# Kernel tuning notes

Hardware: AMD Instinct MI355X
Metric: run time of the kernel (lower is better)

The kernel has to match this reference:

```python
import jax, jax.numpy as jnp
import numpy as np

N = 100000
E = 1600000
D = 64        # HID_NODE_ENC == HID_EDGE_ENC
H = 128       # HIDDEN_NODE_ONE
EPS = 1e-5
NEG_SLOPE = 0.01


def _xavier(key, shape):
    fan_in, fan_out = shape[0], shape[1]
    limit = float(np.sqrt(6.0 / (fan_in + fan_out)))
    return jax.random.uniform(key, shape, jnp.float32, -limit, limit)


def setup_inputs() -> dict:
    key = jax.random.key(0)
    ks = jax.random.split(key, 10)
    x = jax.random.normal(ks[0], (N, D), jnp.float32)
    edge_index = jax.random.randint(ks[1], (2, E), 0, N, jnp.int64)
    edge_attr = jax.random.normal(ks[2], (E, D), jnp.float32)
    u = jax.random.normal(ks[3], (1, 16), jnp.float32)
    batch = jnp.zeros((N,), jnp.int64)
    b_init = jnp.float32(0.01)
    params = {
        # node_mlp_1: Lin(128->128), LeakyReLU, BN(128), Lin(128->128)
        "W1": _xavier(ks[4], (2 * D, H)), "b1": jnp.full((H,), b_init),
        "g1": jnp.ones((H,), jnp.float32), "be1": jnp.zeros((H,), jnp.float32),
        "W2": _xavier(ks[5], (H, H)), "b2": jnp.full((H,), b_init),
        # node_mlp_2: Lin(192->128), LeakyReLU, BN(128), Lin(128->64)
        "W3": _xavier(ks[6], (H + D, H)), "b3": jnp.full((H,), b_init),
        "g2": jnp.ones((H,), jnp.float32), "be2": jnp.zeros((H,), jnp.float32),
        "W4": _xavier(ks[7], (H, D)), "b4": jnp.full((D,), b_init),
    }
    return {"x": x, "edge_index": edge_index, "edge_attr": edge_attr,
            "u": u, "batch": batch, **params}


def _bn(h, gamma, beta):
    # BatchNorm1d in training mode: biased batch statistics
    mean = jnp.mean(h, axis=0)
    var = jnp.mean(jnp.square(h - mean), axis=0)
    return (h - mean) * jax.lax.rsqrt(var + EPS) * gamma + beta


def reference(x, edge_index, edge_attr, u, batch,
              W1, b1, g1, be1, W2, b2,
              W3, b3, g2, be2, W4, b4):
    row, col = edge_index[0], edge_index[1]
    # gather + concat: [E, 2D]
    h = jnp.concatenate([x[row], edge_attr], axis=1)
    # node_mlp_1
    h = jax.nn.leaky_relu(h @ W1 + b1, NEG_SLOPE)
    h = _bn(h, g1, be1)
    h = h @ W2 + b2                       # [E, H]
    # scatter_add by destination node
    agg = jax.ops.segment_sum(h, col, num_segments=x.shape[0])  # [N, H]
    # concat with node feats, node_mlp_2
    h2 = jnp.concatenate([x, agg], axis=1)  # [N, H+D]
    h2 = jax.nn.leaky_relu(h2 @ W3 + b3, NEG_SLOPE)
    h2 = _bn(h2, g2, be2)
    return h2 @ W4 + b4                    # [N, D]
```

## Files before the change

### kernel.cpp

```cpp
#include <hip/hip_runtime.h>

#define NN 100000
#define NE 1600000
#define NTILE_E (NE / 128)
#define NTILE_N 782

typedef __attribute__((ext_vector_type(4))) float f32x4;
typedef __attribute__((ext_vector_type(8))) short s16x8;

__device__ __forceinline__ unsigned short f2bf(float f) {
  unsigned u = __builtin_bit_cast(unsigned, f);
  u = (u + 0x7FFFu + ((u >> 16) & 1u)) >> 16;
  return (unsigned short)u;
}
__device__ __forceinline__ void pack4(float4 v, unsigned short* dst) {
  ushort4 h;
  h.x = f2bf(v.x); h.y = f2bf(v.y); h.z = f2bf(v.z); h.w = f2bf(v.w);
  *(ushort4*)dst = h;
}

__global__ void k0_prep(const float* __restrict__ W1, const float* __restrict__ W3,
                        unsigned short* __restrict__ W1bT, unsigned short* __restrict__ W3bT) {
  int i = blockIdx.x * 256 + threadIdx.x;
  if (i < 16384) {
    int n = i >> 7, k = i & 127;
    W1bT[i] = f2bf(W1[k * 128 + n]);
  } else if (i < 16384 + 24576) {
    int j = i - 16384;
    int n = j / 192, k = j % 192;
    W3bT[j] = f2bf(W3[k * 128 + n]);
  }
}

__global__ void k_hist(const int* __restrict__ eidx, int* __restrict__ hist) {
  int e = blockIdx.x * 256 + threadIdx.x;
  if (e < NE) atomicAdd(&hist[eidx[NE + e]], 1);
}

__global__ void k_scan(int* __restrict__ hist, float* __restrict__ cntF) {
  __shared__ int ssum[1024];
  const int t = threadIdx.x;
  const int base = t * 98;
  const int cl = (base >= NN) ? 0 : ((NN - base < 98) ? (NN - base) : 98);
  int s = 0;
  for (int i = 0; i < cl; i++) s += hist[base + i];
  ssum[t] = s;
  __syncthreads();
  for (int d = 1; d < 1024; d <<= 1) {
    int v = (t >= d) ? ssum[t - d] : 0;
    __syncthreads();
    ssum[t] += v;
    __syncthreads();
  }
  int run = (t == 0) ? 0 : ssum[t - 1];
  for (int i = 0; i < cl; i++) {
    int hv = hist[base + i];
    hist[base + i] = run;
    cntF[base + i] = (float)hv;
    run += hv;
  }
}

__global__ void k_scatter(const int* __restrict__ eidx, int* __restrict__ off,
                          int* __restrict__ colS, int* __restrict__ eaIdx) {
  int e = blockIdx.x * 256 + threadIdx.x;
  if (e < NE) {
    int c = eidx[NE + e];
    int p = atomicAdd(&off[c], 1);
    colS[p] = c;
    eaIdx[p] = e;
  }
}

__global__ __launch_bounds__(256, 2) void k1_edge(
    const float* __restrict__ x, const int* __restrict__ eidx,
    const float* __restrict__ ea, const unsigned short* __restrict__ W1bT,
    const float* __restrict__ b1, const int* __restrict__ colS,
    const int* __restrict__ eaIdx,
    float* __restrict__ S, float* __restrict__ stat1) {
  __shared__ __align__(16) unsigned short At[128][136];
  __shared__ __align__(16) float Hs1[128][68];
  __shared__ int rIdxS[128];
  __shared__ int eIdxS[128];
  __shared__ int colT[132];
  __shared__ float sred[256];
  float (*Hs0)[68] = (float (*)[68])At;

  const int tid = threadIdx.x;
  const int wave = tid >> 6, lane = tid & 63;
  const int l15 = lane & 15, quad = lane >> 4;
  const int rowbase = (wave >> 1) * 64;
  const int colbase = (wave & 1) * 64;

  s16x8 bfrag[4][4];
#pragma unroll
  for (int ct = 0; ct < 4; ct++)
#pragma unroll
    for (int ks = 0; ks < 4; ks++)
      bfrag[ct][ks] = *(const s16x8*)(W1bT + (colbase + ct * 16 + l15) * 128 + ks * 32 + quad * 8);

  float b1j[4];
#pragma unroll
  for (int ct = 0; ct < 4; ct++) b1j[ct] = b1[colbase + ct * 16 + l15];

  float lsum[4] = {0, 0, 0, 0}, lsq[4] = {0, 0, 0, 0};

  for (int tile = blockIdx.x; tile < NTILE_E; tile += gridDim.x) {
    const int eb = tile * 128;
    __syncthreads();
    if (tid < 128) {
      int e0 = eaIdx[eb + tid];
      eIdxS[tid] = e0;
      rIdxS[tid] = eidx[e0];
      colT[tid + 1] = colS[eb + tid];
    } else if (tid == 128) {
      colT[0] = (eb > 0) ? colS[eb - 1] : -1;
    } else if (tid == 129) {
      colT[129] = (eb + 128 < NE) ? colS[eb + 128] : -1;
    }
    __syncthreads();
#pragma unroll
    for (int i = 0; i < 8; i++) {
      int idx = tid + i * 256; int e = idx >> 4, c = idx & 15;
      float4 v = ((const float4*)x)[(size_t)rIdxS[e] * 16 + c];
      pack4(v, &At[e][c * 4]);
    }
#pragma unroll
    for (int i = 0; i < 8; i++) {
      int idx = tid + i * 256; int e = idx >> 4, c = idx & 15;
      float4 v = ((const float4*)ea)[(size_t)eIdxS[e] * 16 + c];
      pack4(v, &At[e][64 + c * 4]);
    }
    __syncthreads();

    f32x4 acc[4][4];
#pragma unroll
    for (int rt = 0; rt < 4; rt++)
#pragma unroll
      for (int ct = 0; ct < 4; ct++) acc[rt][ct] = (f32x4){0.f, 0.f, 0.f, 0.f};

#pragma unroll
    for (int ks = 0; ks < 4; ks++) {
      s16x8 af[4];
#pragma unroll
      for (int rt = 0; rt < 4; rt++)
        af[rt] = *(const s16x8*)&At[rowbase + rt * 16 + l15][ks * 32 + quad * 8];
#pragma unroll
      for (int rt = 0; rt < 4; rt++)
#pragma unroll
        for (int ct = 0; ct < 4; ct++)
          acc[rt][ct] = __builtin_amdgcn_mfma_f32_16x16x32_bf16(af[rt], bfrag[ct][ks], acc[rt][ct], 0, 0, 0);
    }

    __syncthreads();
    {
      float (*H)[68] = (wave & 1) ? Hs1 : Hs0;
#pragma unroll
      for (int rt = 0; rt < 4; rt++)
#pragma unroll
        for (int r = 0; r < 4; r++) {
          const int er = rowbase + rt * 16 + quad * 4 + r;
#pragma unroll
          for (int ct = 0; ct < 4; ct++) {
            float v = acc[rt][ct][r] + b1j[ct];
            v = v > 0.0f ? v : 0.01f * v;
            lsum[ct] += v; lsq[ct] += v * v;
            H[er][ct * 16 + l15] = v;
          }
        }
    }
    __syncthreads();

    {
      const int col = tid & 63;
      const int r0 = (tid >> 6) * 32;
#pragma unroll
      for (int h = 0; h < 2; h++) {
        float (*H)[68] = h ? Hs1 : Hs0;
        float runsum = H[r0][col];
        int runstart = r0;
        int curnode = colT[r0 + 1];
        for (int r = r0 + 1; r < r0 + 32; ++r) {
          int nd = colT[r + 1];
          float v = H[r][col];
          if (nd == curnode) { runsum += v; }
          else {
            float* p = S + (size_t)curnode * 128 + h * 64 + col;
            if (colT[runstart] != curnode) *p = runsum;
            else atomicAdd(p, runsum);
            curnode = nd; runsum = v; runstart = r;
          }
        }
        float* p = S + (size_t)curnode * 128 + h * 64 + col;
        if (colT[runstart] != curnode && colT[r0 + 33] != curnode) *p = runsum;
        else atomicAdd(p, runsum);
      }
    }
  }

  sred[tid] = 0.0f;
  __syncthreads();
#pragma unroll
  for (int ct = 0; ct < 4; ct++) {
    float s = lsum[ct], q = lsq[ct];
    s += __shfl_down(s, 32); q += __shfl_down(q, 32);
    s += __shfl_down(s, 16); q += __shfl_down(q, 16);
    if (lane < 16) {
      atomicAdd(&sred[colbase + ct * 16 + l15], s);
      atomicAdd(&sred[128 + colbase + ct * 16 + l15], q);
    }
  }
  __syncthreads();
  atomicAdd(&stat1[tid], sred[tid]);
}

__global__ void k2_fold1(const float* __restrict__ stat1, const float* __restrict__ g1,
                         const float* __restrict__ be1, const float* __restrict__ W2,
                         const float* __restrict__ b2,
                         unsigned short* __restrict__ W2pT, float* __restrict__ v128) {
  __shared__ float s1s[128], t1s[128];
  __shared__ float red[256];
  const int tid = threadIdx.x;
  if (tid < 128) {
    float mean = stat1[tid] * (1.0f / NE);
    float var = stat1[128 + tid] * (1.0f / NE) - mean * mean;
    float rstd = rsqrtf(var + 1e-5f);
    float s = g1[tid] * rstd;
    s1s[tid] = s; t1s[tid] = be1[tid] - mean * s;
  }
  __syncthreads();
  const int b = blockIdx.x;
  if (b < 16) {
#pragma unroll
    for (int j = 0; j < 4; j++) {
      int i = b * 1024 + j * 256 + tid;
      int k = i >> 7, n = i & 127;
      W2pT[n * 128 + k] = f2bf(s1s[k] * W2[i]);
    }
  } else {
    int j = tid & 127, hh = tid >> 7;
    float p = 0.f;
    for (int k = hh * 64; k < hh * 64 + 64; k++) p += t1s[k] * W2[k * 128 + j];
    red[tid] = p;
    __syncthreads();
    if (tid < 128) v128[tid] = red[tid] + red[tid + 128] + b2[tid];
  }
}

__global__ __launch_bounds__(256, 2) void k3_node(
    const float* __restrict__ x, const float* __restrict__ S, const float* __restrict__ cnt,
    const unsigned short* __restrict__ W2pT, const float* __restrict__ v128,
    const unsigned short* __restrict__ W3bT, const float* __restrict__ b3,
    unsigned short* __restrict__ tOut, float* __restrict__ stat2) {
  __shared__ unsigned short Abuf[128][136];
  __shared__ unsigned short Xbuf[128][72];
  __shared__ float cbuf[128];
  __shared__ float sred[256];

  const int tid = threadIdx.x;
  const int wave = tid >> 6, lane = tid & 63;
  const int l15 = lane & 15, quad = lane >> 4;
  const int rowbase = (wave >> 1) * 64;
  const int colbase = (wave & 1) * 64;

  float vj[4], b3j[4];
#pragma unroll
  for (int ct = 0; ct < 4; ct++) {
    int jc = colbase + ct * 16 + l15;
    vj[ct] = v128[jc]; b3j[ct] = b3[jc];
  }
  float lsum[4] = {0, 0, 0, 0}, lsq[4] = {0, 0, 0, 0};

  for (int t = blockIdx.x; t < NTILE_N; t += gridDim.x) {
    const int nb = t * 128;
    __syncthreads();
#pragma unroll
    for (int i = 0; i < 16; i++) {
      int idx = tid + i * 256; int e = idx >> 5, c = idx & 31;
      int node = nb + e;
      float4 v = {0.f, 0.f, 0.f, 0.f};
      if (node < NN) v = ((const float4*)S)[(size_t)node * 32 + c];
      pack4(v, &Abuf[e][c * 4]);
    }
#pragma unroll
    for (int i = 0; i < 8; i++) {
      int idx = tid + i * 256; int e = idx >> 4, c = idx & 15;
      int node = nb + e;
      float4 v = {0.f, 0.f, 0.f, 0.f};
      if (node < NN) v = ((const float4*)x)[(size_t)node * 16 + c];
      pack4(v, &Xbuf[e][c * 4]);
    }
    if (tid < 128) cbuf[tid] = (nb + tid < NN) ? cnt[nb + tid] : 0.0f;
    __syncthreads();

    f32x4 acc[4][4];
#pragma unroll
    for (int rt = 0; rt < 4; rt++)
#pragma unroll
      for (int ct = 0; ct < 4; ct++) acc[rt][ct] = (f32x4){0.f, 0.f, 0.f, 0.f};
#pragma unroll
    for (int ks = 0; ks < 4; ks++) {
      s16x8 af[4];
#pragma unroll
      for (int rt = 0; rt < 4; rt++)
        af[rt] = *(const s16x8*)&Abuf[rowbase + rt * 16 + l15][ks * 32 + quad * 8];
      s16x8 bfr[4];
#pragma unroll
      for (int ct = 0; ct < 4; ct++)
        bfr[ct] = *(const s16x8*)(W2pT + (colbase + ct * 16 + l15) * 128 + ks * 32 + quad * 8);
#pragma unroll
      for (int rt = 0; rt < 4; rt++)
#pragma unroll
        for (int ct = 0; ct < 4; ct++)
          acc[rt][ct] = __builtin_amdgcn_mfma_f32_16x16x32_bf16(af[rt], bfr[ct], acc[rt][ct], 0, 0, 0);
    }
    __syncthreads();
#pragma unroll
    for (int rt = 0; rt < 4; rt++)
#pragma unroll
      for (int r = 0; r < 4; r++) {
        int er = rowbase + rt * 16 + quad * 4 + r;
#pragma unroll
        for (int ct = 0; ct < 4; ct++) {
          float val = acc[rt][ct][r] + cbuf[er] * vj[ct];
          Abuf[er][colbase + ct * 16 + l15] = f2bf(val);
        }
      }
    __syncthreads();

    f32x4 acc2[4][4];
#pragma unroll
    for (int rt = 0; rt < 4; rt++)
#pragma unroll
      for (int ct = 0; ct < 4; ct++) acc2[rt][ct] = (f32x4){0.f, 0.f, 0.f, 0.f};
#pragma unroll
    for (int ks = 0; ks < 6; ks++) {
      s16x8 af[4];
      if (ks < 2) {
#pragma unroll
        for (int rt = 0; rt < 4; rt++)
          af[rt] = *(const s16x8*)&Xbuf[rowbase + rt * 16 + l15][ks * 32 + quad * 8];
      } else {
#pragma unroll
        for (int rt = 0; rt < 4; rt++)
          af[rt] = *(const s16x8*)&Abuf[rowbase + rt * 16 + l15][(ks - 2) * 32 + quad * 8];
      }
      s16x8 bfr[4];
#pragma unroll
      for (int ct = 0; ct < 4; ct++)
        bfr[ct] = *(const s16x8*)(W3bT + (size_t)(colbase + ct * 16 + l15) * 192 + ks * 32 + quad * 8);
#pragma unroll
      for (int rt = 0; rt < 4; rt++)
#pragma unroll
        for (int ct = 0; ct < 4; ct++)
          acc2[rt][ct] = __builtin_amdgcn_mfma_f32_16x16x32_bf16(af[rt], bfr[ct], acc2[rt][ct], 0, 0, 0);
    }

#pragma unroll
    for (int rt = 0; rt < 4; rt++)
#pragma unroll
      for (int r = 0; r < 4; r++) {
        int er = rowbase + rt * 16 + quad * 4 + r;
        int node = nb + er;
        if (node < NN) {
#pragma unroll
          for (int ct = 0; ct < 4; ct++) {
            float val = acc2[rt][ct][r] + b3j[ct];
            val = val > 0.0f ? val : 0.01f * val;
            lsum[ct] += val; lsq[ct] += val * val;
            tOut[(size_t)node * 128 + colbase + ct * 16 + l15] = f2bf(val);
          }
        }
      }
  }

  sred[tid] = 0.0f;
  __syncthreads();
#pragma unroll
  for (int ct = 0; ct < 4; ct++) {
    float s = lsum[ct], q = lsq[ct];
    s += __shfl_down(s, 32); q += __shfl_down(q, 32);
    s += __shfl_down(s, 16); q += __shfl_down(q, 16);
    if (lane < 16) {
      atomicAdd(&sred[colbase + ct * 16 + l15], s);
      atomicAdd(&sred[128 + colbase + ct * 16 + l15], q);
    }
  }
  __syncthreads();
  atomicAdd(&stat2[tid], sred[tid]);
}

__global__ void k5_fold2(const float* __restrict__ stat2, const float* __restrict__ g2,
                         const float* __restrict__ be2, const float* __restrict__ W4,
                         const float* __restrict__ b4,
                         unsigned short* __restrict__ W4fT, float* __restrict__ b4f) {
  __shared__ float s2s[128], t2s[128];
  __shared__ float red[256];
  const int tid = threadIdx.x;
  if (tid < 128) {
    float mean = stat2[tid] * (1.0f / NN);
    float var = stat2[128 + tid] * (1.0f / NN) - mean * mean;
    float rstd = rsqrtf(var + 1e-5f);
    float s = g2[tid] * rstd;
    s2s[tid] = s; t2s[tid] = be2[tid] - mean * s;
  }
  __syncthreads();
  const int b = blockIdx.x;
  if (b < 8) {
#pragma unroll
    for (int j = 0; j < 4; j++) {
      int i = b * 1024 + j * 256 + tid;
      int k = i >> 6, n = i & 63;
      W4fT[n * 128 + k] = f2bf(s2s[k] * W4[i]);
    }
  } else {
    int j = tid & 63, part = tid >> 6;
    float p = 0.f;
    for (int k = part * 32; k < part * 32 + 32; k++) p += t2s[k] * W4[k * 64 + j];
    red[tid] = p;
    __syncthreads();
    if (tid < 64) b4f[tid] = red[tid] + red[tid + 64] + red[tid + 128] + red[tid + 192] + b4[tid];
  }
}

__global__ __launch_bounds__(256, 2) void k6_out(
    const unsigned short* __restrict__ tIn, const unsigned short* __restrict__ W4fT,
    const float* __restrict__ b4f, float* __restrict__ out) {
  __shared__ unsigned short Abuf[128][136];
  const int tid = threadIdx.x;
  const int wave = tid >> 6, lane = tid & 63;
  const int l15 = lane & 15, quad = lane >> 4;
  const int rowbase = (wave >> 1) * 64;
  const int colbase = (wave & 1) * 32;

  s16x8 bfrag[2][4];
#pragma unroll
  for (int ct = 0; ct < 2; ct++)
#pragma unroll
    for (int ks = 0; ks < 4; ks++)
      bfrag[ct][ks] = *(const s16x8*)(W4fT + (colbase + ct * 16 + l15) * 128 + ks * 32 + quad * 8);
  float bj[2];
#pragma unroll
  for (int ct = 0; ct < 2; ct++) bj[ct] = b4f[colbase + ct * 16 + l15];

  for (int t = blockIdx.x; t < NTILE_N; t += gridDim.x) {
    const int nb = t * 128;
    __syncthreads();
#pragma unroll
    for (int i = 0; i < 8; i++) {
      int idx = tid + i * 256; int e = idx >> 4, c = idx & 15;
      int node = nb + e;
      s16x8 v = {0, 0, 0, 0, 0, 0, 0, 0};
      if (node < NN) v = *(const s16x8*)(tIn + (size_t)node * 128 + c * 8);
      *(s16x8*)&Abuf[e][c * 8] = v;
    }
    __syncthreads();

    f32x4 acc[4][2];
#pragma unroll
    for (int rt = 0; rt < 4; rt++)
#pragma unroll
      for (int ct = 0; ct < 2; ct++) acc[rt][ct] = (f32x4){0.f, 0.f, 0.f, 0.f};
#pragma unroll
    for (int ks = 0; ks < 4; ks++) {
      s16x8 af[4];
#pragma unroll
      for (int rt = 0; rt < 4; rt++)
        af[rt] = *(const s16x8*)&Abuf[rowbase + rt * 16 + l15][ks * 32 + quad * 8];
#pragma unroll
      for (int rt = 0; rt < 4; rt++)
#pragma unroll
        for (int ct = 0; ct < 2; ct++)
          acc[rt][ct] = __builtin_amdgcn_mfma_f32_16x16x32_bf16(af[rt], bfrag[ct][ks], acc[rt][ct], 0, 0, 0);
    }
#pragma unroll
    for (int rt = 0; rt < 4; rt++)
#pragma unroll
      for (int r = 0; r < 4; r++) {
        int er = rowbase + rt * 16 + quad * 4 + r;
        int node = nb + er;
        if (node < NN) {
#pragma unroll
          for (int ct = 0; ct < 2; ct++)
            out[(size_t)node * 64 + colbase + ct * 16 + l15] = acc[rt][ct][r] + bj[ct];
        }
      }
  }
}

extern "C" void kernel_launch(void* const* d_in, const int* in_sizes, int n_in,
                              void* d_out, int out_size, void* d_ws, size_t ws_size,
                              hipStream_t stream) {
  (void)in_sizes; (void)n_in; (void)out_size; (void)ws_size;
  const float* x   = (const float*)d_in[0];
  const int*   ei  = (const int*)d_in[1];
  const float* ea  = (const float*)d_in[2];
  const float* W1  = (const float*)d_in[5];
  const float* b1  = (const float*)d_in[6];
  const float* g1  = (const float*)d_in[7];
  const float* be1 = (const float*)d_in[8];
  const float* W2  = (const float*)d_in[9];
  const float* b2  = (const float*)d_in[10];
  const float* W3  = (const float*)d_in[11];
  const float* b3  = (const float*)d_in[12];
  const float* g2  = (const float*)d_in[13];
  const float* be2 = (const float*)d_in[14];
  const float* W4  = (const float*)d_in[15];
  const float* b4  = (const float*)d_in[16];
  float* out = (float*)d_out;

  char* w = (char*)d_ws;
  float* S     = (float*)(w);
  float* stat1 = (float*)(w + 51200000);
  float* stat2 = (float*)(w + 51201024);
  int*   hist  = (int*)  (w + 51202048);
  float* cntF  = (float*)(w + 51602432);
  unsigned short* W1bT = (unsigned short*)(w + 52002816);
  unsigned short* W3bT = (unsigned short*)(w + 52035584);
  unsigned short* W2pT = (unsigned short*)(w + 52084736);
  float* v128  = (float*)(w + 52117504);
  unsigned short* W4fT = (unsigned short*)(w + 52118016);
  float* b4f   = (float*)(w + 52134400);
  unsigned short* tOut = (unsigned short*)(w + 52134656);
  int* colS  = (int*)(w + 52134656);
  int* eaIdx = (int*)(w + 58534656);

  hipMemsetAsync(d_ws, 0, 51602432, stream);

  k0_prep<<<160, 256, 0, stream>>>(W1, W3, W1bT, W3bT);
  k_hist<<<6250, 256, 0, stream>>>(ei, hist);
  k_scan<<<1, 1024, 0, stream>>>(hist, cntF);
  k_scatter<<<6250, 256, 0, stream>>>(ei, hist, colS, eaIdx);
  k1_edge<<<512, 256, 0, stream>>>(x, ei, ea, W1bT, b1, colS, eaIdx, S, stat1);
  k2_fold1<<<17, 256, 0, stream>>>(stat1, g1, be1, W2, b2, W2pT, v128);
  k3_node<<<512, 256, 0, stream>>>(x, S, cntF, W2pT, v128, W3bT, b3, tOut, stat2);
  k5_fold2<<<9, 256, 0, stream>>>(stat2, g2, be2, W4, b4, W4fT, b4f);
  k6_out<<<512, 256, 0, stream>>>(tOut, W4fT, b4f, out);
}
```

Before: 1.223 ms.

## Pre-convert x to bf16, pack edge records, parallelize scan, shrink edge LDS

Converts x to bf16 once in a prep kernel so the edge and node kernels gather half the bytes with no per-tile packing. The sorted edge metadata (dest, edge id, source) is packed into one int4 record per edge, which removes the dependent load of the source index. The single-block prefix scan becomes a three-kernel multi-block scan. The edge kernel reuses one LDS buffer for both column halves, with extra barriers, so it can run three blocks per CU on a larger grid. The cost is an extra bf16 buffer write and more kernel launches.

```diff
diff --git a/kernel.cpp b/kernel.cpp
--- a/kernel.cpp
+++ b/kernel.cpp
@@ -4,6 +4,7 @@
 #define NE 1600000
 #define NTILE_E (NE / 128)
 #define NTILE_N 782
+#define SCAN_B 98
 
 typedef __attribute__((ext_vector_type(4))) float f32x4;
 typedef __attribute__((ext_vector_type(8))) short s16x8;
@@ -19,14 +20,20 @@
   *(ushort4*)dst = h;
 }
 
-__global__ void k0_prep(const float* __restrict__ W1, const float* __restrict__ W3,
-                        unsigned short* __restrict__ W1bT, unsigned short* __restrict__ W3bT) {
-  int i = blockIdx.x * 256 + threadIdx.x;
-  if (i < 16384) {
-    int n = i >> 7, k = i & 127;
-    W1bT[i] = f2bf(W1[k * 128 + n]);
-  } else if (i < 16384 + 24576) {
-    int j = i - 16384;
+__global__ void k_prep(const float* __restrict__ x, const float* __restrict__ W1,
+                       const float* __restrict__ W3, unsigned short* __restrict__ xb,
+                       unsigned short* __restrict__ W1bT, unsigned short* __restrict__ W3bT) {
+  int t = blockIdx.x * 256 + threadIdx.x;
+  if (t < 1600000) {
+    float4 v = ((const float4*)x)[t];
+    ushort4 h; h.x = f2bf(v.x); h.y = f2bf(v.y); h.z = f2bf(v.z); h.w = f2bf(v.w);
+    ((ushort4*)xb)[t] = h;
+  }
+  if (t < 16384) {
+    int n = t >> 7, k = t & 127;
+    W1bT[t] = f2bf(W1[k * 128 + n]);
+  } else if (t < 16384 + 24576) {
+    int j = t - 16384;
     int n = j / 192, k = j % 192;
     W3bT[j] = f2bf(W3[k * 128 + n]);
   }
@@ -37,54 +44,84 @@
   if (e < NE) atomicAdd(&hist[eidx[NE + e]], 1);
 }
 
-__global__ void k_scan(int* __restrict__ hist, float* __restrict__ cntF) {
-  __shared__ int ssum[1024];
-  const int t = threadIdx.x;
-  const int base = t * 98;
-  const int cl = (base >= NN) ? 0 : ((NN - base < 98) ? (NN - base) : 98);
+__global__ void k_scanA(const int* __restrict__ hist, int* __restrict__ bsum) {
+  __shared__ int red[256];
+  int t = threadIdx.x, b = blockIdx.x;
+  int i0 = b * 1024 + t * 4;
   int s = 0;
-  for (int i = 0; i < cl; i++) s += hist[base + i];
-  ssum[t] = s;
-  __syncthreads();
-  for (int d = 1; d < 1024; d <<= 1) {
-    int v = (t >= d) ? ssum[t - d] : 0;
-    __syncthreads();
-    ssum[t] += v;
-    __syncthreads();
-  }
-  int run = (t == 0) ? 0 : ssum[t - 1];
-  for (int i = 0; i < cl; i++) {
-    int hv = hist[base + i];
-    hist[base + i] = run;
-    cntF[base + i] = (float)hv;
-    run += hv;
-  }
+  if (i0 + 3 < NN) { int4 v = *(const int4*)(hist + i0); s = v.x + v.y + v.z + v.w; }
+  else { for (int j = 0; j < 4; j++) if (i0 + j < NN) s += hist[i0 + j]; }
+  red[t] = s;
+  __syncthreads();
+  for (int d = 128; d > 0; d >>= 1) { if (t < d) red[t] += red[t + d]; __syncthreads(); }
+  if (t == 0) bsum[b] = red[0];
+}
+
+__global__ void k_scanB(int* __restrict__ bsum) {
+  __shared__ int s[128];
+  int t = threadIdx.x;
+  s[t] = (t < SCAN_B) ? bsum[t] : 0;
+  __syncthreads();
+  for (int d = 1; d < 128; d <<= 1) {
+    int v = (t >= d) ? s[t - d] : 0;
+    __syncthreads();
+    s[t] += v;
+    __syncthreads();
+  }
+  if (t < SCAN_B) bsum[t] = (t == 0) ? 0 : s[t - 1];
+}
+
+__global__ void k_scanC(int* __restrict__ hist, const int* __restrict__ bsum,
+                        float* __restrict__ cntF) {
+  __shared__ int red[256];
+  int t = threadIdx.x, b = blockIdx.x;
+  int i0 = b * 1024 + t * 4;
+  int h0 = 0, h1 = 0, h2 = 0, h3 = 0;
+  if (i0 + 3 < NN) { int4 v = *(const int4*)(hist + i0); h0 = v.x; h1 = v.y; h2 = v.z; h3 = v.w; }
+  else {
+    if (i0 < NN) h0 = hist[i0];
+    if (i0 + 1 < NN) h1 = hist[i0 + 1];
+    if (i0 + 2 < NN) h2 = hist[i0 + 2];
+    if (i0 + 3 < NN) h3 = hist[i0 + 3];
+  }
+  int s = h0 + h1 + h2 + h3;
+  red[t] = s;
+  __syncthreads();
+  for (int d = 1; d < 256; d <<= 1) {
+    int v = (t >= d) ? red[t - d] : 0;
+    __syncthreads();
+    red[t] += v;
+    __syncthreads();
+  }
+  int excl = bsum[b] + red[t] - s;
+  if (i0 < NN)     { hist[i0] = excl;     cntF[i0] = (float)h0;     excl += h0; }
+  if (i0 + 1 < NN) { hist[i0 + 1] = excl; cntF[i0 + 1] = (float)h1; excl += h1; }
+  if (i0 + 2 < NN) { hist[i0 + 2] = excl; cntF[i0 + 2] = (float)h2; excl += h2; }
+  if (i0 + 3 < NN) { hist[i0 + 3] = excl; cntF[i0 + 3] = (float)h3; excl += h3; }
 }
 
 __global__ void k_scatter(const int* __restrict__ eidx, int* __restrict__ off,
-                          int* __restrict__ colS, int* __restrict__ eaIdx) {
+                          int4* __restrict__ rec) {
   int e = blockIdx.x * 256 + threadIdx.x;
   if (e < NE) {
+    int r = eidx[e];
     int c = eidx[NE + e];
     int p = atomicAdd(&off[c], 1);
-    colS[p] = c;
-    eaIdx[p] = e;
-  }
-}
-
-__global__ __launch_bounds__(256, 2) void k1_edge(
-    const float* __restrict__ x, const int* __restrict__ eidx,
-    const float* __restrict__ ea, const unsigned short* __restrict__ W1bT,
-    const float* __restrict__ b1, const int* __restrict__ colS,
-    const int* __restrict__ eaIdx,
+    rec[p] = make_int4(c, e, r, 0);
+  }
+}
+
+__global__ __launch_bounds__(256, 3) void k1_edge(
+    const unsigned short* __restrict__ xb, const float* __restrict__ ea,
+    const unsigned short* __restrict__ W1bT, const float* __restrict__ b1,
+    const int4* __restrict__ rec,
     float* __restrict__ S, float* __restrict__ stat1) {
   __shared__ __align__(16) unsigned short At[128][136];
-  __shared__ __align__(16) float Hs1[128][68];
+  __shared__ int eIdxS[128];
   __shared__ int rIdxS[128];
-  __shared__ int eIdxS[128];
   __shared__ int colT[132];
   __shared__ float sred[256];
-  float (*Hs0)[68] = (float (*)[68])At;
+  float (*H)[68] = (float (*)[68])At;
 
   const int tid = threadIdx.x;
   const int wave = tid >> 6, lane = tid & 63;
@@ -109,21 +146,18 @@
     const int eb = tile * 128;
     __syncthreads();
     if (tid < 128) {
-      int e0 = eaIdx[eb + tid];
-      eIdxS[tid] = e0;
-      rIdxS[tid] = eidx[e0];
-      colT[tid + 1] = colS[eb + tid];
+      int4 rc = rec[eb + tid];
+      colT[tid + 1] = rc.x; eIdxS[tid] = rc.y; rIdxS[tid] = rc.z;
     } else if (tid == 128) {
-      colT[0] = (eb > 0) ? colS[eb - 1] : -1;
+      colT[0] = (eb > 0) ? rec[eb - 1].x : -1;
     } else if (tid == 129) {
-      colT[129] = (eb + 128 < NE) ? colS[eb + 128] : -1;
-    }
-    __syncthreads();
-#pragma unroll
-    for (int i = 0; i < 8; i++) {
-      int idx = tid + i * 256; int e = idx >> 4, c = idx & 15;
-      float4 v = ((const float4*)x)[(size_t)rIdxS[e] * 16 + c];
-      pack4(v, &At[e][c * 4]);
+      colT[129] = (eb + 128 < NE) ? rec[eb + 128].x : -1;
+    }
+    __syncthreads();
+#pragma unroll
+    for (int i = 0; i < 4; i++) {
+      int idx = tid + i * 256; int e = idx >> 3, c = idx & 7;
+      *(s16x8*)&At[e][c * 8] = *(const s16x8*)(xb + (size_t)rIdxS[e] * 64 + c * 8);
     }
 #pragma unroll
     for (int i = 0; i < 8; i++) {
@@ -152,31 +186,28 @@
           acc[rt][ct] = __builtin_amdgcn_mfma_f32_16x16x32_bf16(af[rt], bfrag[ct][ks], acc[rt][ct], 0, 0, 0);
     }
 
-    __syncthreads();
-    {
-      float (*H)[68] = (wave & 1) ? Hs1 : Hs0;
-#pragma unroll
-      for (int rt = 0; rt < 4; rt++)
-#pragma unroll
-        for (int r = 0; r < 4; r++) {
-          const int er = rowbase + rt * 16 + quad * 4 + r;
-#pragma unroll
-          for (int ct = 0; ct < 4; ct++) {
-            float v = acc[rt][ct][r] + b1j[ct];
-            v = v > 0.0f ? v : 0.01f * v;
-            lsum[ct] += v; lsq[ct] += v * v;
-            H[er][ct * 16 + l15] = v;
+#pragma unroll
+    for (int h = 0; h < 2; h++) {
+      __syncthreads();
+      if ((wave & 1) == h) {
+#pragma unroll
+        for (int rt = 0; rt < 4; rt++)
+#pragma unroll
+          for (int r = 0; r < 4; r++) {
+            const int er = rowbase + rt * 16 + quad * 4 + r;
+#pragma unroll
+            for (int ct = 0; ct < 4; ct++) {
+              float v = acc[rt][ct][r] + b1j[ct];
+              v = v > 0.0f ? v : 0.01f * v;
+              lsum[ct] += v; lsq[ct] += v * v;
+              H[er][ct * 16 + l15] = v;
+            }
           }
-        }
-    }
-    __syncthreads();
-
-    {
-      const int col = tid & 63;
-      const int r0 = (tid >> 6) * 32;
-#pragma unroll
-      for (int h = 0; h < 2; h++) {
-        float (*H)[68] = h ? Hs1 : Hs0;
+      }
+      __syncthreads();
+      {
+        const int col = tid & 63;
+        const int r0 = (tid >> 6) * 32;
         float runsum = H[r0][col];
         int runstart = r0;
         int curnode = colT[r0 + 1];
@@ -248,7 +279,8 @@
 }
 
 __global__ __launch_bounds__(256, 2) void k3_node(
-    const float* __restrict__ x, const float* __restrict__ S, const float* __restrict__ cnt,
+    const unsigned short* __restrict__ xb, const float* __restrict__ S,
+    const float* __restrict__ cnt,
     const unsigned short* __restrict__ W2pT, const float* __restrict__ v128,
     const unsigned short* __restrict__ W3bT, const float* __restrict__ b3,
     unsigned short* __restrict__ tOut, float* __restrict__ stat2) {
@@ -283,12 +315,12 @@
       pack4(v, &Abuf[e][c * 4]);
     }
 #pragma unroll
-    for (int i = 0; i < 8; i++) {
-      int idx = tid + i * 256; int e = idx >> 4, c = idx & 15;
+    for (int i = 0; i < 4; i++) {
+      int idx = tid + i * 256; int e = idx >> 3, c = idx & 7;
       int node = nb + e;
-      float4 v = {0.f, 0.f, 0.f, 0.f};
-      if (node < NN) v = ((const float4*)x)[(size_t)node * 16 + c];
-      pack4(v, &Xbuf[e][c * 4]);
+      s16x8 v = {0, 0, 0, 0, 0, 0, 0, 0};
+      if (node < NN) v = *(const s16x8*)(xb + (size_t)node * 64 + c * 8);
+      *(s16x8*)&Xbuf[e][c * 8] = v;
     }
     if (tid < 128) cbuf[tid] = (nb + tid < NN) ? cnt[nb + tid] : 0.0f;
     __syncthreads();
@@ -513,27 +545,30 @@
   float* S     = (float*)(w);
   float* stat1 = (float*)(w + 51200000);
   float* stat2 = (float*)(w + 51201024);
-  int*   hist  = (int*)  (w + 51202048);
-  float* cntF  = (float*)(w + 51602432);
-  unsigned short* W1bT = (unsigned short*)(w + 52002816);
-  unsigned short* W3bT = (unsigned short*)(w + 52035584);
-  unsigned short* W2pT = (unsigned short*)(w + 52084736);
-  float* v128  = (float*)(w + 52117504);
-  unsigned short* W4fT = (unsigned short*)(w + 52118016);
-  float* b4f   = (float*)(w + 52134400);
-  unsigned short* tOut = (unsigned short*)(w + 52134656);
-  int* colS  = (int*)(w + 52134656);
-  int* eaIdx = (int*)(w + 58534656);
-
-  hipMemsetAsync(d_ws, 0, 51602432, stream);
-
-  k0_prep<<<160, 256, 0, stream>>>(W1, W3, W1bT, W3bT);
+  int*   bsum  = (int*)  (w + 51202048);
+  int*   hist  = (int*)  (w + 51202560);
+  float* cntF  = (float*)(w + 51602944);
+  unsigned short* W1bT = (unsigned short*)(w + 52003328);
+  unsigned short* W3bT = (unsigned short*)(w + 52036096);
+  unsigned short* W2pT = (unsigned short*)(w + 52085248);
+  float* v128  = (float*)(w + 52118016);
+  unsigned short* W4fT = (unsigned short*)(w + 52118528);
+  float* b4f   = (float*)(w + 52134912);
+  unsigned short* xb16 = (unsigned short*)(w + 52135168);
+  unsigned short* tOut = (unsigned short*)(w + 64935168);
+  int4* rec = (int4*)(w + 64935168);
+
+  hipMemsetAsync(d_ws, 0, 51602944, stream);
+
+  k_prep<<<6250, 256, 0, stream>>>(x, W1, W3, xb16, W1bT, W3bT);
   k_hist<<<6250, 256, 0, stream>>>(ei, hist);
-  k_scan<<<1, 1024, 0, stream>>>(hist, cntF);
-  k_scatter<<<6250, 256, 0, stream>>>(ei, hist, colS, eaIdx);
-  k1_edge<<<512, 256, 0, stream>>>(x, ei, ea, W1bT, b1, colS, eaIdx, S, stat1);
+  k_scanA<<<SCAN_B, 256, 0, stream>>>(hist, bsum);
+  k_scanB<<<1, 128, 0, stream>>>(bsum);
+  k_scanC<<<SCAN_B, 256, 0, stream>>>(hist, bsum, cntF);
+  k_scatter<<<6250, 256, 0, stream>>>(ei, hist, rec);
+  k1_edge<<<1024, 256, 0, stream>>>(xb16, ea, W1bT, b1, rec, S, stat1);
   k2_fold1<<<17, 256, 0, stream>>>(stat1, g1, be1, W2, b2, W2pT, v128);
-  k3_node<<<512, 256, 0, stream>>>(x, S, cntF, W2pT, v128, W3bT, b3, tOut, stat2);
+  k3_node<<<512, 256, 0, stream>>>(xb16, S, cntF, W2pT, v128, W3bT, b3, tOut, stat2);
   k5_fold2<<<9, 256, 0, stream>>>(stat2, g2, be2, W4, b4, W4fT, b4f);
   k6_out<<<512, 256, 0, stream>>>(tOut, W4fT, b4f, out);
 }
```

Result: slower. 1.567 ms (+28.2%).
